# Kernel tuning notes

Measured on AMD Instinct MI355X. Metric: run time of the kernel, lower is better.

## Reference

```python
import jax, jax.numpy as jnp
import numpy as np


def setup_inputs() -> dict:
    key = jax.random.key(0)
    k1, k2 = jax.random.split(key)
    B, N, M, D = 8, 4096, 4096, 3
    return {
        "input": jax.random.normal(k1, (B, N, D), dtype=jnp.float32),
        "target": jax.random.normal(k2, (B, M, D), dtype=jnp.float32),
    }


def reference(input, target):
    x2 = jnp.sum(input * input, axis=-1)          # [B, N]
    y2 = jnp.sum(target * target, axis=-1)        # [B, M]
    xy = jnp.einsum("bnd,bmd->bnm", input, target)  # [B, N, M]
    sqdist = x2[:, :, None] + y2[:, None, :] - 2.0 * xy
    sqdist = jnp.maximum(sqdist, 0.0)  # clamp numerical negatives
    sqdist1 = jnp.min(sqdist, axis=2)  # nearest target for each input point [B, N]
    sqdist2 = jnp.min(sqdist, axis=1)  # nearest input for each target point [B, M]
    return jnp.mean(sqdist1) + jnp.mean(sqdist2)
```

## Files before the change

### kernel.cpp

```cpp
#include <hip/hip_runtime.h>
#include <math.h>

#define BATCH  8
#define NPTS   4096
#define TPB    256
#define QPT    4
#define QCHUNK (TPB * QPT)
#define NQC    (NPTS / QCHUNK)
#define NCC    16
#define CTILE  (NPTS / NCC)

__global__ __launch_bounds__(TPB) void chamfer_min_kernel(
    const float* __restrict__ input,
    const float* __restrict__ target,
    unsigned int* __restrict__ best)
{
    const int dir = blockIdx.z;
    const int b   = blockIdx.y;
    const int qc  = blockIdx.x & (NQC - 1);
    const int cc  = blockIdx.x >> 2;

    const float* __restrict__ qp = (dir ? target : input) + (size_t)b * NPTS * 3;
    const float* __restrict__ cp = (dir ? input  : target) + (size_t)b * NPTS * 3;

    __shared__ float4 cand[CTILE];
    {
        const int c = cc * CTILE + threadIdx.x;
        const float cx = cp[3 * c + 0];
        const float cy = cp[3 * c + 1];
        const float cz = cp[3 * c + 2];
        cand[threadIdx.x] = make_float4(-2.0f * cx, -2.0f * cy, -2.0f * cz,
                                        fmaf(cx, cx, fmaf(cy, cy, cz * cz)));
    }

    const int q0 = qc * QCHUNK + (int)threadIdx.x * QPT;
    float px[QPT], py[QPT], pz[QPT], pmin[QPT];
    #pragma unroll
    for (int k = 0; k < QPT; ++k) {
        px[k] = qp[3 * (q0 + k) + 0];
        py[k] = qp[3 * (q0 + k) + 1];
        pz[k] = qp[3 * (q0 + k) + 2];
        pmin[k] = 3.4e38f;
    }
    __syncthreads();

    #pragma unroll 4
    for (int m = 0; m < CTILE; ++m) {
        const float4 c = cand[m];
        #pragma unroll
        for (int k = 0; k < QPT; ++k) {
            const float t = fmaf(px[k], c.x,
                            fmaf(py[k], c.y,
                            fmaf(pz[k], c.z, c.w)));
            pmin[k] = fminf(pmin[k], t);
        }
    }

    unsigned int* bq = best + ((size_t)(dir * BATCH + b)) * NPTS + q0;
    #pragma unroll
    for (int k = 0; k < QPT; ++k) {
        const float x2 = fmaf(px[k], px[k], fmaf(py[k], py[k], pz[k] * pz[k]));
        const float v  = fmaxf(pmin[k] + x2, 0.0f);
        atomicMin(&bq[k], __float_as_uint(v));
    }
}

__global__ __launch_bounds__(TPB) void chamfer_reduce_kernel(
    const unsigned int* __restrict__ best, float* __restrict__ out)
{
    const int i = (blockIdx.x * TPB + (int)threadIdx.x) * 4;
    const uint4 u = *(const uint4*)(best + i);
    float s = __uint_as_float(u.x) + __uint_as_float(u.y) +
              __uint_as_float(u.z) + __uint_as_float(u.w);
    #pragma unroll
    for (int off = 32; off > 0; off >>= 1)
        s += __shfl_down(s, off, 64);

    __shared__ float wsum[TPB / 64];
    if ((threadIdx.x & 63) == 0) wsum[threadIdx.x >> 6] = s;
    __syncthreads();
    if (threadIdx.x == 0) {
        const float t = wsum[0] + wsum[1] + wsum[2] + wsum[3];
        atomicAdd(out, t * (1.0f / (float)(BATCH * NPTS)));
    }
}

extern "C" void kernel_launch(void* const* d_in, const int* in_sizes, int n_in,
                              void* d_out, int out_size, void* d_ws, size_t ws_size,
                              hipStream_t stream) {
    const float* input  = (const float*)d_in[0];
    const float* target = (const float*)d_in[1];
    float* out = (float*)d_out;
    unsigned int* best = (unsigned int*)d_ws;

    hipMemsetAsync(best, 0x7F, (size_t)2 * BATCH * NPTS * sizeof(unsigned int), stream);
    hipMemsetAsync(out, 0, sizeof(float), stream);

    dim3 grid1(NQC * NCC, BATCH, 2);
    chamfer_min_kernel<<<grid1, dim3(TPB), 0, stream>>>(input, target, best);

    dim3 grid2((2 * BATCH * NPTS) / (TPB * 4));
    chamfer_reduce_kernel<<<grid2, dim3(TPB), 0, stream>>>(best, out);
}
```

Baseline: 82.64 us.

## Replace atomicMin with per-chunk partial minima, raise points per thread

Each thread now handles 8 query points instead of 4, loaded with float4 vector reads, and candidate chunks double to 32. Per-chunk minima go to a partial buffer with plain vector stores instead of atomicMin, which also removes the 0x7F memset. The reduce kernel takes the minimum across the 32 partials before summing. This trades atomic contention and one memset for more workspace traffic, and the larger per-thread tile raises register pressure.

New measurement: 81.86 us. Within noise of the previous version (-0.9%).

```diff
diff --git a/kernel.cpp b/kernel.cpp
--- a/kernel.cpp
+++ b/kernel.cpp
@@ -4,27 +4,27 @@
 #define BATCH  8
 #define NPTS   4096
 #define TPB    256
-#define QPT    4
+#define QPT    8
 #define QCHUNK (TPB * QPT)
 #define NQC    (NPTS / QCHUNK)
-#define NCC    16
+#define NCC    32
 #define CTILE  (NPTS / NCC)
 
 __global__ __launch_bounds__(TPB) void chamfer_min_kernel(
     const float* __restrict__ input,
     const float* __restrict__ target,
-    unsigned int* __restrict__ best)
+    float* __restrict__ part)
 {
     const int dir = blockIdx.z;
     const int b   = blockIdx.y;
     const int qc  = blockIdx.x & (NQC - 1);
-    const int cc  = blockIdx.x >> 2;
+    const int cc  = blockIdx.x >> 1;
 
     const float* __restrict__ qp = (dir ? target : input) + (size_t)b * NPTS * 3;
     const float* __restrict__ cp = (dir ? input  : target) + (size_t)b * NPTS * 3;
 
     __shared__ float4 cand[CTILE];
-    {
+    if (threadIdx.x < CTILE) {
         const int c = cc * CTILE + threadIdx.x;
         const float cx = cp[3 * c + 0];
         const float cy = cp[3 * c + 1];
@@ -34,17 +34,25 @@
     }
 
     const int q0 = qc * QCHUNK + (int)threadIdx.x * QPT;
+    float v[3 * QPT];
+    const float4* __restrict__ qv = (const float4*)(qp + 3 * q0);
+    #pragma unroll
+    for (int i = 0; i < 6; ++i) {
+        const float4 t = qv[i];
+        v[4 * i + 0] = t.x; v[4 * i + 1] = t.y;
+        v[4 * i + 2] = t.z; v[4 * i + 3] = t.w;
+    }
     float px[QPT], py[QPT], pz[QPT], pmin[QPT];
     #pragma unroll
     for (int k = 0; k < QPT; ++k) {
-        px[k] = qp[3 * (q0 + k) + 0];
-        py[k] = qp[3 * (q0 + k) + 1];
-        pz[k] = qp[3 * (q0 + k) + 2];
+        px[k] = v[3 * k + 0];
+        py[k] = v[3 * k + 1];
+        pz[k] = v[3 * k + 2];
         pmin[k] = 3.4e38f;
     }
     __syncthreads();
 
-    #pragma unroll 4
+    #pragma unroll 8
     for (int m = 0; m < CTILE; ++m) {
         const float4 c = cand[m];
         #pragma unroll
@@ -56,22 +64,33 @@
         }
     }
 
-    unsigned int* bq = best + ((size_t)(dir * BATCH + b)) * NPTS + q0;
+    float res[QPT];
     #pragma unroll
     for (int k = 0; k < QPT; ++k) {
         const float x2 = fmaf(px[k], px[k], fmaf(py[k], py[k], pz[k] * pz[k]));
-        const float v  = fmaxf(pmin[k] + x2, 0.0f);
-        atomicMin(&bq[k], __float_as_uint(v));
+        res[k] = fmaxf(pmin[k] + x2, 0.0f);
     }
+    float* o = part + (((size_t)(dir * BATCH + b) * NCC + cc) * NPTS + q0);
+    *(float4*)(o + 0) = make_float4(res[0], res[1], res[2], res[3]);
+    *(float4*)(o + 4) = make_float4(res[4], res[5], res[6], res[7]);
 }
 
 __global__ __launch_bounds__(TPB) void chamfer_reduce_kernel(
-    const unsigned int* __restrict__ best, float* __restrict__ out)
+    const float* __restrict__ part, float* __restrict__ out)
 {
     const int i = (blockIdx.x * TPB + (int)threadIdx.x) * 4;
-    const uint4 u = *(const uint4*)(best + i);
-    float s = __uint_as_float(u.x) + __uint_as_float(u.y) +
-              __uint_as_float(u.z) + __uint_as_float(u.w);
+    const int g = i >> 12;
+    const int q = i & (NPTS - 1);
+    const float* __restrict__ p = part + ((size_t)g * NCC) * NPTS + q;
+
+    float4 mn = *(const float4*)p;
+    #pragma unroll 8
+    for (int cc = 1; cc < NCC; ++cc) {
+        const float4 t = *(const float4*)(p + (size_t)cc * NPTS);
+        mn.x = fminf(mn.x, t.x); mn.y = fminf(mn.y, t.y);
+        mn.z = fminf(mn.z, t.z); mn.w = fminf(mn.w, t.w);
+    }
+    float s = mn.x + mn.y + mn.z + mn.w;
     #pragma unroll
     for (int off = 32; off > 0; off >>= 1)
         s += __shfl_down(s, off, 64);
@@ -90,15 +109,14 @@
                               hipStream_t stream) {
     const float* input  = (const float*)d_in[0];
     const float* target = (const float*)d_in[1];
-    float* out = (float*)d_out;
-    unsigned int* best = (unsigned int*)d_ws;
+    float* out  = (float*)d_out;
+    float* part = (float*)d_ws;
 
-    hipMemsetAsync(best, 0x7F, (size_t)2 * BATCH * NPTS * sizeof(unsigned int), stream);
     hipMemsetAsync(out, 0, sizeof(float), stream);
 
     dim3 grid1(NQC * NCC, BATCH, 2);
-    chamfer_min_kernel<<<grid1, dim3(TPB), 0, stream>>>(input, target, best);
+    chamfer_min_kernel<<<grid1, dim3(TPB), 0, stream>>>(input, target, part);
 
     dim3 grid2((2 * BATCH * NPTS) / (TPB * 4));
-    chamfer_reduce_kernel<<<grid2, dim3(TPB), 0, stream>>>(best, out);
+    chamfer_reduce_kernel<<<grid2, dim3(TPB), 0, stream>>>(part, out);
 }
```
